# Optimization experiments

Measured on AMD Instinct MI355X. Metric: run time of the kernel, lower is better.

The kernel has to match this reference:

```python
import jax, jax.numpy as jnp
import numpy as np

N, H, R, E = 100000, 128, 30, 600000
EPS = 1e-5  # BatchNorm1d default eps


def _rgcn_layer(h, src, dst, etype, W, root, bias):
    """PyG RGCNConv: out = h @ root + bias + sum_r scatter_mean_r(h[src] @ W[r]).
    Mean is per (dst, relation) edge count."""
    n = h.shape[0]
    r_count = W.shape[0]
    seg = dst * r_count + etype                      # combined (dst, rel) segment id
    deg = jax.ops.segment_sum(jnp.ones_like(etype, dtype=h.dtype), seg,
                              num_segments=n * r_count)
    norm = 1.0 / jnp.maximum(deg[seg], 1.0)          # (E,) per-edge mean weight

    def body(out, inp):
        Wr, r = inp
        xr = h @ Wr                                  # (N,H) relation-transformed feats
        contrib = jnp.where((etype == r)[:, None], xr[src] * norm[:, None], 0.0)
        return out + jax.ops.segment_sum(contrib, dst, num_segments=n), None

    out0 = h @ root + bias
    out, _ = jax.lax.scan(body, out0, (W, jnp.arange(r_count)))
    return out


def _bn_relu(h, gamma, beta):
    # BatchNorm1d in training mode: biased batch statistics over the node dim
    mu = h.mean(axis=0)
    var = h.var(axis=0)
    return jax.nn.relu((h - mu) * jax.lax.rsqrt(var + EPS) * gamma + beta)


def setup_inputs() -> dict:
    key = jax.random.key(0)
    ks = jax.random.split(key, 16)
    s = 1.0 / np.sqrt(H)
    return {
        "x": jnp.arange(N, dtype=jnp.int32),
        "edge_index": jax.random.randint(ks[0], (2, E), 0, N, dtype=jnp.int32),
        "edge_type": jax.random.randint(ks[1], (E,), 0, R, dtype=jnp.int32),
        "emb": jax.random.normal(ks[2], (N, H), jnp.float32) * s,
        "W1": jax.random.normal(ks[3], (R, H, H), jnp.float32) * s,
        "root1": jax.random.normal(ks[4], (H, H), jnp.float32) * s,
        "b1": jnp.zeros((H,), jnp.float32),
        "g1": jnp.ones((H,), jnp.float32),
        "be1": jnp.zeros((H,), jnp.float32),
        "W2": jax.random.normal(ks[5], (R, H, H), jnp.float32) * s,
        "root2": jax.random.normal(ks[6], (H, H), jnp.float32) * s,
        "b2": jnp.zeros((H,), jnp.float32),
        "g2": jnp.ones((H,), jnp.float32),
        "be2": jnp.zeros((H,), jnp.float32),
    }


def reference(x, edge_index, edge_type, emb, W1, root1, b1, g1, be1,
              W2, root2, b2, g2, be2):
    src, dst = edge_index[0], edge_index[1]
    h = emb[x]                                        # (N,H) embedding lookup
    h = _bn_relu(_rgcn_layer(h, src, dst, edge_type, W1, root1, b1), g1, be1)
    h = _bn_relu(_rgcn_layer(h, src, dst, edge_type, W2, root2, b2), g2, be2)
    return h  # dropout is identity (deterministic reference)
```

## Files before the change

### kernel.cpp

```cpp
#include <hip/hip_runtime.h>
#include <hip/hip_bf16.h>

#define NN 100000
#define HH 128
#define RR 30
#define RR2 15
#define NE 600000
#define TILE 64
#define CH 64
#define EPAD (NE + RR * TILE)
#define NCHMAX (EPAD / TILE)
#define NB_PS ((NN + 255) / 256)
#define NBLK_BN 784
#define RPB_BN 128
#define BN_EPS 1e-5f

typedef __bf16 v8bf __attribute__((ext_vector_type(8)));
typedef float  v4f  __attribute__((ext_vector_type(4)));
typedef unsigned int v4u __attribute__((ext_vector_type(4)));

static __device__ __forceinline__ unsigned short f2b(float f) {
    unsigned int u = __float_as_uint(f);
    unsigned int r = (u + 0x7FFF + ((u >> 16) & 1)) >> 16;
    return (unsigned short)r;
}

static __device__ __forceinline__ unsigned int pk_bf16(float lo, float hi) {
    unsigned int r;
    asm("v_cvt_pk_bf16_f32 %0, %1, %2" : "=v"(r) : "v"(lo), "v"(hi));
    return r;
}

__global__ void k_hist(const int* __restrict__ dst, const int* __restrict__ et,
                       unsigned int* __restrict__ deg16, int* __restrict__ cnt) {
    __shared__ int lh[RR];
    int t = threadIdx.x;
    if (t < RR) lh[t] = 0;
    __syncthreads();
    int i = blockIdx.x * blockDim.x + t;
    if (i < NE) {
        int d = dst[i], r = et[i];
        atomicAdd(&deg16[(size_t)d * RR2 + (r >> 1)], 1u << ((r & 1) * 16));
        atomicAdd(&lh[r], 1);
    }
    __syncthreads();
    if (t < RR && lh[t]) atomicAdd(&cnt[t], lh[t]);
}

__global__ void k_degsum(const unsigned int* __restrict__ deg16,
                         int* __restrict__ cnt_d) {
    int d = blockIdx.x * blockDim.x + threadIdx.x;
    if (d >= NN) return;
    int s = 0;
#pragma unroll
    for (int r2 = 0; r2 < RR2; ++r2) {
        unsigned int v = deg16[(size_t)d * RR2 + r2];
        s += (int)(v & 0xffffu) + (int)(v >> 16);
    }
    cnt_d[d] = s;
}

__global__ void k_scan(const int* __restrict__ cnt, int* __restrict__ cursor,
                       int* __restrict__ totals,
                       int* __restrict__ src_s, int* __restrict__ dst_s,
                       float* __restrict__ norm_s, int* __restrict__ dpos_s,
                       int* __restrict__ chunk_rel, int need_dst) {
    __shared__ int off[RR + 1];
    if (threadIdx.x == 0) {
        int acc = 0;
        for (int r = 0; r < RR; ++r) {
            off[r] = acc;
            acc += (cnt[r] + TILE - 1) / TILE;
        }
        off[RR] = acc;
        totals[0] = acc * TILE;
    }
    __syncthreads();
    for (int r = 0; r < RR; ++r) {
        for (int c = off[r] + (int)threadIdx.x; c < off[r + 1]; c += blockDim.x)
            chunk_rel[c] = r;
        int begin = off[r] * TILE + cnt[r];
        int end   = off[r + 1] * TILE;
        for (int p = begin + (int)threadIdx.x; p < end; p += blockDim.x) {
            src_s[p] = 0; norm_s[p] = 0.f;
            dpos_s[p] = NE;
            if (need_dst) dst_s[p] = 0;
        }
    }
    if (threadIdx.x == 0)
        for (int r = 0; r < RR; ++r) cursor[r] = off[r] * TILE;
}

__global__ void k_psum1(const int* __restrict__ c, int* __restrict__ bsum) {
    __shared__ int sh[256];
    int i = blockIdx.x * 256 + threadIdx.x;
    sh[threadIdx.x] = (i < NN) ? c[i] : 0;
    __syncthreads();
    for (int s = 128; s > 0; s >>= 1) {
        if (threadIdx.x < s) sh[threadIdx.x] += sh[threadIdx.x + s];
        __syncthreads();
    }
    if (threadIdx.x == 0) bsum[blockIdx.x] = sh[0];
}

__global__ void k_psum2(int* __restrict__ bsum) {
    __shared__ int sh[512];
    int t = threadIdx.x;
    sh[t] = (t < NB_PS) ? bsum[t] : 0;
    __syncthreads();
    if (t == 0) {
        int acc = 0;
        for (int b = 0; b < NB_PS; ++b) { int v = sh[b]; sh[b] = acc; acc += v; }
    }
    __syncthreads();
    if (t < NB_PS) bsum[t] = sh[t];
}

__global__ void k_psum3(const int* __restrict__ c, const int* __restrict__ bscan,
                        int* __restrict__ off, int* __restrict__ cur) {
    __shared__ int sh[256];
    int t = threadIdx.x;
    int i = blockIdx.x * 256 + t;
    int v = (i < NN) ? c[i] : 0;
    sh[t] = v;
    __syncthreads();
    for (int s = 1; s < 256; s <<= 1) {
        int a = (t >= s) ? sh[t - s] : 0;
        __syncthreads();
        sh[t] += a;
        __syncthreads();
    }
    int excl = sh[t] - v + bscan[blockIdx.x];
    if (i < NN) { off[i] = excl; cur[i] = excl; }
    if (i == 0) off[NN] = NE;
}

__global__ void k_fillds2(const int* __restrict__ off, int* __restrict__ ds2) {
    int d = blockIdx.x * blockDim.x + threadIdx.x;
    if (d >= NN) return;
    int s = off[d], e = off[d + 1];
    for (int p = s; p < e; ++p) ds2[p] = d;
}

__global__ void k_scatter(const int* __restrict__ src, const int* __restrict__ dst,
                          const int* __restrict__ et,
                          const unsigned int* __restrict__ deg16,
                          int* __restrict__ cursor, int* __restrict__ cursor_dst,
                          int* __restrict__ src_s, int* __restrict__ dst_s,
                          float* __restrict__ norm_s, int* __restrict__ dpos_s,
                          int need_dst) {
    __shared__ int lh[RR];
    __shared__ int lbase[RR];
    int t = threadIdx.x;
    if (t < RR) lh[t] = 0;
    __syncthreads();
    int i = blockIdx.x * blockDim.x + t;
    int r = 0, d = 0, lrank = 0;
    bool valid = (i < NE);
    if (valid) {
        r = et[i]; d = dst[i];
        lrank = atomicAdd(&lh[r], 1);
    }
    __syncthreads();
    if (t < RR && lh[t]) lbase[t] = atomicAdd(&cursor[t], lh[t]);
    __syncthreads();
    if (valid) {
        int pos = lbase[r] + lrank;
        src_s[pos] = src[i];
        if (need_dst) dst_s[pos] = d;
        int dg = (int)((deg16[(size_t)d * RR2 + (r >> 1)] >> ((r & 1) * 16)) & 0xffffu);
        norm_s[pos] = 1.0f / (float)(dg > 1 ? dg : 1);
        dpos_s[pos] = atomicAdd(&cursor_dst[d], 1);
    }
}

__global__ void k_convW(const float* __restrict__ W, unsigned short* __restrict__ Wt,
                        int total) {
    int idx = blockIdx.x * blockDim.x + threadIdx.x;
    if (idx >= total) return;
    int m = idx / (HH * HH);
    int rem = idx % (HH * HH);
    int k = rem / HH, c = rem % HH;
    Wt[m * HH * HH + c * HH + k] = f2b(W[idx]);
}

__global__ void k_embed(const int* __restrict__ x, const float* __restrict__ emb,
                        unsigned int* __restrict__ hb2) {
    int idx = blockIdx.x * blockDim.x + threadIdx.x;
    if (idx >= NN * HH / 2) return;
    int i = idx >> 6;
    int j2 = (idx & 63) * 2;
    const float* p = emb + (size_t)x[i] * HH + j2;
    hb2[idx] = pk_bf16(p[0], p[1]);
}

__global__ __launch_bounds__(256) void k_rootgemm(const unsigned short* __restrict__ hb,
                                                  const unsigned short* __restrict__ rootT,
                                                  const float* __restrict__ bias,
                                                  float* __restrict__ tmp) {
    __shared__ __align__(16) unsigned short Xs[TILE][HH + 8];
    __shared__ __align__(16) unsigned short Ws[HH][HH + 8];
    int base = blockIdx.x * TILE;
    int t = threadIdx.x;

    {
        int l = t >> 2, lr = t & 3;
        int row = base + l;
        for (int i = 0; i < 4; ++i) {
            int g = lr + 4 * i;
            uint4 v = {0u, 0u, 0u, 0u};
            if (row < NN) v = *reinterpret_cast<const uint4*>(hb + (size_t)row * HH + g * 8);
            *reinterpret_cast<uint4*>(&Xs[l][g * 8]) = v;
        }
    }
    for (int i = 0; i < 8; ++i) {
        int idx = t + 256 * i;
        int row = idx >> 4, g = idx & 15;
        *reinterpret_cast<uint4*>(&Ws[row][g * 8]) =
            *reinterpret_cast<const uint4*>(rootT + row * HH + g * 8);
    }
    __syncthreads();

    int w = t >> 6, lane = t & 63;
    int lr16 = lane & 15, kg = lane >> 4;
    v4f acc[8];
    for (int n = 0; n < 8; ++n) acc[n] = (v4f){0.f, 0.f, 0.f, 0.f};
#pragma unroll
    for (int kk = 0; kk < 4; ++kk) {
        int k0 = kk * 32 + kg * 8;
        v8bf a = *reinterpret_cast<const v8bf*>(&Xs[w * 16 + lr16][k0]);
#pragma unroll
        for (int n = 0; n < 8; ++n) {
            v8bf b = *reinterpret_cast<const v8bf*>(&Ws[n * 16 + lr16][k0]);
            acc[n] = __builtin_amdgcn_mfma_f32_16x16x32_bf16(a, b, acc[n], 0, 0, 0);
        }
    }
#pragma unroll
    for (int n = 0; n < 8; ++n)
        for (int j = 0; j < 4; ++j) {
            int row = base + w * 16 + kg * 4 + j;
            int col = n * 16 + lr16;
            if (row < NN) tmp[(size_t)row * HH + col] = acc[n][j] + bias[col];
        }
}

__global__ __launch_bounds__(256) void k_edgegemm_x(const unsigned short* __restrict__ hb,
                                                    const unsigned short* __restrict__ Wt,
                                                    const int* __restrict__ src_s,
                                                    const int* __restrict__ chunk_rel,
                                                    const float* __restrict__ norm_s,
                                                    const int* __restrict__ dpos_s,
                                                    const int* __restrict__ totals,
                                                    unsigned short* __restrict__ xe) {
    int ebase = blockIdx.x * TILE;
    if (ebase >= totals[0]) return;
    __shared__ __align__(16) unsigned short S[HH * (HH + 8)];
    int t = threadIdx.x;
    int rel = chunk_rel[blockIdx.x];

    const unsigned short* Wr = Wt + (size_t)rel * HH * HH;
    for (int i = 0; i < 8; ++i) {
        int idx = t + 256 * i;
        int row = idx >> 4, g = idx & 15;
        *reinterpret_cast<uint4*>(&S[row * (HH + 8) + g * 8]) =
            *reinterpret_cast<const uint4*>(Wr + row * HH + g * 8);
    }

    int w = t >> 6, lane = t & 63;
    int lr16 = lane & 15, kg = lane >> 4;
    int slot = w * 16 + lr16;
    int srow = src_s[ebase + slot];
    float nrm = norm_s[ebase + slot];

    v8bf xf[4];
    const unsigned short* hrow = hb + (size_t)srow * HH + kg * 8;
#pragma unroll
    for (int kk = 0; kk < 4; ++kk)
        xf[kk] = *reinterpret_cast<const v8bf*>(hrow + kk * 32);

    __syncthreads();

    v4f acc[8];
#pragma unroll
    for (int n = 0; n < 8; ++n) acc[n] = (v4f){0.f, 0.f, 0.f, 0.f};
#pragma unroll
    for (int n = 0; n < 8; ++n)
#pragma unroll
        for (int kk = 0; kk < 4; ++kk) {
            v8bf wf = *reinterpret_cast<const v8bf*>(
                &S[(n * 16 + lr16) * (HH + 8) + kk * 32 + kg * 8]);
            acc[n] = __builtin_amdgcn_mfma_f32_16x16x32_bf16(wf, xf[kk], acc[n], 0, 0, 0);
        }

    __syncthreads();

    int c = slot & 7;
#pragma unroll
    for (int n = 0; n < 8; ++n) {
        unsigned int w0 = pk_bf16(acc[n][0] * nrm, acc[n][1] * nrm);
        unsigned int w1 = pk_bf16(acc[n][2] * nrm, acc[n][3] * nrm);
        unsigned long long p = (unsigned long long)w0 | ((unsigned long long)w1 << 32);
        int a = n * 4 + kg;
        int sw = (((a >> 1) ^ c) << 1) | (a & 1);
        *reinterpret_cast<unsigned long long*>(&S[slot * HH + sw * 4]) = p;
    }
    __syncthreads();
    {
        int l = t >> 2, lr = t & 3;
        size_t drow = (size_t)dpos_s[ebase + l];
        int cs = l & 7;
        unsigned short* orow = xe + drow * HH;
#pragma unroll
        for (int i = 0; i < 4; ++i) {
            int j = lr + 4 * i;
            v4u v = *reinterpret_cast<const v4u*>(&S[l * HH + (j ^ cs) * 8]);
            *reinterpret_cast<v4u*>(orow + j * 8) = v;
        }
    }
}

__global__ __launch_bounds__(256) void k_edgegemm_at(const unsigned short* __restrict__ hb,
                                                     const unsigned short* __restrict__ Wt,
                                                     const int* __restrict__ src_s,
                                                     const int* __restrict__ dst_s,
                                                     const int* __restrict__ chunk_rel,
                                                     const float* __restrict__ norm_s,
                                                     const int* __restrict__ totals,
                                                     float* __restrict__ tmp) {
    int ebase = blockIdx.x * TILE;
    if (ebase >= totals[0]) return;
    __shared__ __align__(16) unsigned short Xs[TILE][HH + 8];
    __shared__ __align__(16) unsigned short Ws[HH][HH + 8];
    __shared__ int   src_l[TILE];
    __shared__ int   dst_l[TILE];
    __shared__ float nrm_l[TILE];
    int t = threadIdx.x;
    if (t < TILE) {
        src_l[t] = src_s[ebase + t];
        dst_l[t] = dst_s[ebase + t];
        nrm_l[t] = norm_s[ebase + t];
    }
    int rel = chunk_rel[blockIdx.x];
    __syncthreads();
    {
        int l = t >> 2, lr = t & 3;
        int srow = src_l[l];
        for (int i = 0; i < 4; ++i) {
            int g = lr + 4 * i;
            *reinterpret_cast<uint4*>(&Xs[l][g * 8]) =
                *reinterpret_cast<const uint4*>(hb + (size_t)srow * HH + g * 8);
        }
    }
    const unsigned short* Wr = Wt + (size_t)rel * HH * HH;
    for (int i = 0; i < 8; ++i) {
        int idx = t + 256 * i;
        int row = idx >> 4, g = idx & 15;
        *reinterpret_cast<uint4*>(&Ws[row][g * 8]) =
            *reinterpret_cast<const uint4*>(Wr + row * HH + g * 8);
    }
    __syncthreads();
    int w = t >> 6, lane = t & 63;
    int lr16 = lane & 15, kg = lane >> 4;
    v4f acc[8];
    for (int n = 0; n < 8; ++n) acc[n] = (v4f){0.f, 0.f, 0.f, 0.f};
#pragma unroll
    for (int kk = 0; kk < 4; ++kk) {
        int k0 = kk * 32 + kg * 8;
        v8bf a = *reinterpret_cast<const v8bf*>(&Xs[w * 16 + lr16][k0]);
#pragma unroll
        for (int n = 0; n < 8; ++n) {
            v8bf b = *reinterpret_cast<const v8bf*>(&Ws[n * 16 + lr16][k0]);
            acc[n] = __builtin_amdgcn_mfma_f32_16x16x32_bf16(a, b, acc[n], 0, 0, 0);
        }
    }
#pragma unroll
    for (int n = 0; n < 8; ++n)
        for (int j = 0; j < 4; ++j) {
            int slot = w * 16 + kg * 4 + j;
            int col  = n * 16 + lr16;
            atomicAdd(&tmp[(size_t)dst_l[slot] * HH + col], acc[n][j] * nrm_l[slot]);
        }
}

__global__ __launch_bounds__(256) void k_aggseg(const unsigned int* __restrict__ xe32,
                                                const int* __restrict__ ds2,
                                                float* __restrict__ tmp) {
    int wid = (blockIdx.x * blockDim.x + threadIdx.x) >> 6;
    int lane = threadIdx.x & 63;
    if (wid >= NE / CH) return;
    int c0 = wid * CH;

    int dme = ds2[c0 + lane];
    int dpre = __shfl_up(dme, 1);
    if (lane == 0) dpre = (c0 == 0) ? -1 : ds2[c0 - 1];
    unsigned long long bmask = __ballot(dme != dpre);
    int dnext = (c0 + CH < NE) ? ds2[c0 + CH] : -1;

    int dcur = __shfl(dme, 0);
    bool fresh = (bmask & 1ull) != 0;
    float a0 = 0.f, a1 = 0.f;
    for (int q0 = 0; q0 < CH; q0 += 16) {
        unsigned int v[16];
#pragma unroll
        for (int j = 0; j < 16; ++j)
            v[j] = xe32[(size_t)(c0 + q0 + j) * 64 + lane];
#pragma unroll
        for (int j = 0; j < 16; ++j) {
            int q = q0 + j;
            if (q && ((bmask >> q) & 1ull)) {
                float* base = tmp + (size_t)dcur * HH + lane * 2;
                if (fresh) {
                    float2* b2 = reinterpret_cast<float2*>(base);
                    float2 o = *b2; o.x += a0; o.y += a1; *b2 = o;
                } else {
                    atomicAdd(base, a0);
                    atomicAdd(base + 1, a1);
                }
                a0 = 0.f; a1 = 0.f;
                dcur = __shfl(dme, q);
                fresh = true;
            }
            a0 += __uint_as_float(v[j] << 16);
            a1 += __uint_as_float(v[j] & 0xffff0000u);
        }
    }
    {
        bool endclean = (dnext != dcur);
        float* base = tmp + (size_t)dcur * HH + lane * 2;
        if (fresh && endclean) {
            float2* b2 = reinterpret_cast<float2*>(base);
            float2 o = *b2; o.x += a0; o.y += a1; *b2 = o;
        } else {
            atomicAdd(base, a0);
            atomicAdd(base + 1, a1);
        }
    }
}

__global__ __launch_bounds__(256) void k_bnsum1(const float* __restrict__ tmp,
                                                float* __restrict__ psum,
                                                float* __restrict__ psq) {
    int t = threadIdx.x;
    int rg = t >> 5, lane = t & 31;
    int base = blockIdx.x * RPB_BN;
    v4f s = {0.f, 0.f, 0.f, 0.f}, q = {0.f, 0.f, 0.f, 0.f};
#pragma unroll 4
    for (int i = 0; i < RPB_BN / 8; ++i) {
        int row = base + rg + 8 * i;
        if (row < NN) {
            v4f v = *reinterpret_cast<const v4f*>(tmp + (size_t)row * HH + lane * 4);
            s += v; q += v * v;
        }
    }
    __shared__ v4f shs[8][32], shq[8][32];
    shs[rg][lane] = s; shq[rg][lane] = q;
    __syncthreads();
    if (rg == 0) {
        v4f ts = shs[0][lane], tq = shq[0][lane];
#pragma unroll
        for (int k = 1; k < 8; ++k) { ts += shs[k][lane]; tq += shq[k][lane]; }
        int b = blockIdx.x;
#pragma unroll
        for (int j = 0; j < 4; ++j) {
            psum[(size_t)(lane * 4 + j) * NBLK_BN + b] = ts[j];
            psq [(size_t)(lane * 4 + j) * NBLK_BN + b] = tq[j];
        }
    }
}

__global__ void k_bnsum2(const float* __restrict__ psum, const float* __restrict__ psq,
                         const float* __restrict__ g, const float* __restrict__ be,
                         float* __restrict__ sc_g, float* __restrict__ shf_g) {
    __shared__ float ssum[HH], ssq[HH];
    int t = threadIdx.x;
    int col = t & 127;
    const float* row = ((t < 128) ? psum : psq) + (size_t)col * NBLK_BN;
    v4f a = {0.f, 0.f, 0.f, 0.f};
    for (int i = 0; i < NBLK_BN / 4; ++i)
        a += *reinterpret_cast<const v4f*>(row + i * 4);
    float acc = a[0] + a[1] + a[2] + a[3];
    if (t < 128) ssum[col] = acc; else ssq[col] = acc;
    __syncthreads();
    if (t < 128) {
        float inv_n = 1.0f / (float)NN;
        float mean = ssum[col] * inv_n;
        float var = ssq[col] * inv_n - mean * mean;
        float sc = g[col] * rsqrtf(var + BN_EPS);
        sc_g[col] = sc;
        shf_g[col] = be[col] - mean * sc;
    }
}

__global__ void k_bnapply(const float* __restrict__ tmp, const float* __restrict__ sc_g,
                          const float* __restrict__ shf_g,
                          unsigned short* __restrict__ hout,
                          float* __restrict__ fout, int write_bf16) {
    int idx = blockIdx.x * blockDim.x + threadIdx.x;
    if (idx >= NN * HH / 4) return;
    int c4 = (idx & 31) * 4;
    v4f v  = *reinterpret_cast<const v4f*>(tmp + (size_t)idx * 4);
    v4f sc = *reinterpret_cast<const v4f*>(sc_g + c4);
    v4f sh = *reinterpret_cast<const v4f*>(shf_g + c4);
    v4f r;
#pragma unroll
    for (int j = 0; j < 4; ++j) r[j] = fmaxf(v[j] * sc[j] + sh[j], 0.f);
    if (write_bf16) {
        uint2 u;
        u.x = pk_bf16(r[0], r[1]);
        u.y = pk_bf16(r[2], r[3]);
        *reinterpret_cast<uint2*>(hout + (size_t)idx * 4) = u;
    } else {
        *reinterpret_cast<v4f*>(fout + (size_t)idx * 4) = r;
    }
}

constexpr size_t OFF_DEG  = 0;
constexpr size_t OFF_HB   = OFF_DEG + (size_t)NN * RR2 * 4;
constexpr size_t OFF_TMP  = OFF_HB + (size_t)NN * HH * 2;
constexpr size_t OFF_W1T  = OFF_TMP + (size_t)NN * HH * 4;
constexpr size_t OFF_W2T  = OFF_W1T + (size_t)RR * HH * HH * 2;
constexpr size_t OFF_R1T  = OFF_W2T + (size_t)RR * HH * HH * 2;
constexpr size_t OFF_R2T  = OFF_R1T + (size_t)HH * HH * 2;
constexpr size_t OFF_SRCS = OFF_R2T + (size_t)HH * HH * 2;
constexpr size_t OFF_DSTS = OFF_SRCS + (size_t)EPAD * 4;
constexpr size_t OFF_NRMS = OFF_DSTS + (size_t)EPAD * 4;
constexpr size_t OFF_DPOS = OFF_NRMS + (size_t)EPAD * 4;
constexpr size_t OFF_DS2  = OFF_DPOS + (size_t)EPAD * 4;
constexpr size_t OFF_CREL = OFF_DS2 + (size_t)EPAD * 4;
constexpr size_t OFF_CNTD = OFF_CREL + ((size_t)NCHMAX * 4 + 255 & ~(size_t)255);
constexpr size_t OFF_OFFD = OFF_CNTD + ((size_t)(NN + 1) * 4 + 255 & ~(size_t)255);
constexpr size_t OFF_CURD = OFF_OFFD + ((size_t)(NN + 1) * 4 + 255 & ~(size_t)255);
constexpr size_t OFF_BSUM = OFF_CURD + ((size_t)NN * 4 + 255 & ~(size_t)255);
constexpr size_t OFF_CTRL = OFF_BSUM + ((size_t)NB_PS * 4 + 255 & ~(size_t)255);
constexpr size_t OFF_SC   = OFF_CTRL + 512;
constexpr size_t OFF_SHF  = OFF_SC + 512;
constexpr size_t OFF_PSUM = OFF_SHF + 512;
constexpr size_t OFF_PSQ  = OFF_PSUM + (size_t)HH * NBLK_BN * 4;
constexpr size_t OFF_XE   = (OFF_PSQ + (size_t)HH * NBLK_BN * 4 + 255) & ~(size_t)255;
constexpr size_t WS_MIN   = OFF_XE;
constexpr size_t WS_FULL  = OFF_XE + (size_t)EPAD * HH * 2;

extern "C" void kernel_launch(void* const* d_in, const int* in_sizes, int n_in,
                              void* d_out, int out_size, void* d_ws, size_t ws_size,
                              hipStream_t stream) {
    const int*   x     = (const int*)d_in[0];
    const int*   eidx  = (const int*)d_in[1];
    const int*   et    = (const int*)d_in[2];
    const float* emb   = (const float*)d_in[3];
    const float* W1    = (const float*)d_in[4];
    const float* root1 = (const float*)d_in[5];
    const float* b1    = (const float*)d_in[6];
    const float* g1    = (const float*)d_in[7];
    const float* be1   = (const float*)d_in[8];
    const float* W2    = (const float*)d_in[9];
    const float* root2 = (const float*)d_in[10];
    const float* b2    = (const float*)d_in[11];
    const float* g2    = (const float*)d_in[12];
    const float* be2   = (const float*)d_in[13];
    float* out = (float*)d_out;

    if (ws_size < WS_MIN) return;
    const bool full = (ws_size >= WS_FULL);
    const int need_dst = full ? 0 : 1;

    char* ws = (char*)d_ws;
    unsigned int* deg16 = (unsigned int*)(ws + OFF_DEG);
    unsigned short* hb = (unsigned short*)(ws + OFF_HB);
    float* tmp    = (float*)(ws + OFF_TMP);
    unsigned short* W1t = (unsigned short*)(ws + OFF_W1T);
    unsigned short* W2t = (unsigned short*)(ws + OFF_W2T);
    unsigned short* r1t = (unsigned short*)(ws + OFF_R1T);
    unsigned short* r2t = (unsigned short*)(ws + OFF_R2T);
    int*   src_s  = (int*)(ws + OFF_SRCS);
    int*   dst_s  = (int*)(ws + OFF_DSTS);
    float* norm_s = (float*)(ws + OFF_NRMS);
    int*   dpos_s = (int*)(ws + OFF_DPOS);
    int*   ds2    = (int*)(ws + OFF_DS2);
    int*   crel   = (int*)(ws + OFF_CREL);
    int*   cnt_d  = (int*)(ws + OFF_CNTD);
    int*   off_d  = (int*)(ws + OFF_OFFD);
    int*   cur_d  = (int*)(ws + OFF_CURD);
    int*   bsum   = (int*)(ws + OFF_BSUM);
    int*   cnt    = (int*)(ws + OFF_CTRL);
    int*   cursor = cnt + 32;
    int*   totals = cnt + 64;
    float* sc_g   = (float*)(ws + OFF_SC);
    float* shf_g  = (float*)(ws + OFF_SHF);
    float* psum   = (float*)(ws + OFF_PSUM);
    float* psq    = (float*)(ws + OFF_PSQ);
    unsigned short* xe = (unsigned short*)(ws + OFF_XE);

    const int* srcp = eidx;
    const int* dstp = eidx + NE;

    hipMemsetAsync(deg16, 0, (size_t)NN * RR2 * 4, stream);
    hipMemsetAsync(cnt, 0, 512, stream);

    k_hist<<<(NE + 255) / 256, 256, 0, stream>>>(dstp, et, deg16, cnt);
    k_degsum<<<(NN + 255) / 256, 256, 0, stream>>>(deg16, cnt_d);
    k_scan<<<1, 256, 0, stream>>>(cnt, cursor, totals, src_s, dst_s, norm_s,
                                  dpos_s, crel, need_dst);
    k_psum1<<<NB_PS, 256, 0, stream>>>(cnt_d, bsum);
    k_psum2<<<1, 512, 0, stream>>>(bsum);
    k_psum3<<<NB_PS, 256, 0, stream>>>(cnt_d, bsum, off_d, cur_d);
    k_fillds2<<<(NN + 255) / 256, 256, 0, stream>>>(off_d, ds2);
    k_scatter<<<(NE + 255) / 256, 256, 0, stream>>>(srcp, dstp, et, deg16, cursor, cur_d,
                                                    src_s, dst_s, norm_s, dpos_s,
                                                    need_dst);
    k_convW<<<(RR * HH * HH + 255) / 256, 256, 0, stream>>>(W1, W1t, RR * HH * HH);
    k_convW<<<(RR * HH * HH + 255) / 256, 256, 0, stream>>>(W2, W2t, RR * HH * HH);
    k_convW<<<(HH * HH + 255) / 256, 256, 0, stream>>>(root1, r1t, HH * HH);
    k_convW<<<(HH * HH + 255) / 256, 256, 0, stream>>>(root2, r2t, HH * HH);
    k_embed<<<(NN * HH / 2 + 255) / 256, 256, 0, stream>>>(x, emb, (unsigned int*)hb);

    const unsigned short* Wts[2] = {W1t, W2t};
    const unsigned short* rts[2] = {r1t, r2t};
    const float* biases[2] = {b1, b2};
    const float* gs[2]     = {g1, g2};
    const float* bes[2]    = {be1, be2};

    const int nchunks = NE / CH;
    for (int layer = 0; layer < 2; ++layer) {
        k_rootgemm<<<(NN + TILE - 1) / TILE, 256, 0, stream>>>(hb, rts[layer],
                                                               biases[layer], tmp);
        if (full) {
            k_edgegemm_x<<<EPAD / TILE, 256, 0, stream>>>(hb, Wts[layer], src_s, crel,
                                                          norm_s, dpos_s, totals, xe);
            k_aggseg<<<(nchunks + 3) / 4, 256, 0, stream>>>((const unsigned int*)xe,
                                                            ds2, tmp);
        } else {
            k_edgegemm_at<<<EPAD / TILE, 256, 0, stream>>>(hb, Wts[layer], src_s, dst_s,
                                                           crel, norm_s, totals, tmp);
        }
        k_bnsum1<<<NBLK_BN, 256, 0, stream>>>(tmp, psum, psq);
        k_bnsum2<<<1, 256, 0, stream>>>(psum, psq, gs[layer], bes[layer], sc_g, shf_g);
        k_bnapply<<<(NN * HH / 4 + 255) / 256, 256, 0, stream>>>(tmp, sc_g, shf_g,
                                                                 hb, out, layer == 0);
    }
}
```

Before: 508.0 us.

## Fuse root GEMM with CSR segment aggregation, removing atomics and ds2 fill

Replaces the separate root GEMM and the atomic segmented aggregation with one kernel. Each block computes the root transform for 64 destination rows with MFMA, then walks each row's CSR range of per-edge transformed features and adds them in registers before a single store with bias. This removes the ds2 fill kernel, one full read-modify-write pass over the fp32 output, and the atomics. The per-row edge loops are serial and uneven in length, and each thread reads strided 8-byte pieces of xe, which may coalesce less well.

Result: faster. 485.2 us (-4.5%).

```diff
diff --git a/kernel.cpp b/kernel.cpp
--- a/kernel.cpp
+++ b/kernel.cpp
@@ -7,7 +7,6 @@
 #define RR2 15
 #define NE 600000
 #define TILE 64
-#define CH 64
 #define EPAD (NE + RR * TILE)
 #define NCHMAX (EPAD / TILE)
 #define NB_PS ((NN + 255) / 256)
@@ -135,13 +134,6 @@
     if (i == 0) off[NN] = NE;
 }
 
-__global__ void k_fillds2(const int* __restrict__ off, int* __restrict__ ds2) {
-    int d = blockIdx.x * blockDim.x + threadIdx.x;
-    if (d >= NN) return;
-    int s = off[d], e = off[d + 1];
-    for (int p = s; p < e; ++p) ds2[p] = d;
-}
-
 __global__ void k_scatter(const int* __restrict__ src, const int* __restrict__ dst,
                           const int* __restrict__ et,
                           const unsigned int* __restrict__ deg16,
@@ -192,6 +184,73 @@
     int j2 = (idx & 63) * 2;
     const float* p = emb + (size_t)x[i] * HH + j2;
     hb2[idx] = pk_bf16(p[0], p[1]);
+}
+
+__global__ __launch_bounds__(256) void k_rootagg(const unsigned short* __restrict__ hb,
+                                                 const unsigned short* __restrict__ rootT,
+                                                 const float* __restrict__ bias,
+                                                 const int* __restrict__ off,
+                                                 const unsigned short* __restrict__ xe,
+                                                 float* __restrict__ tmp) {
+    __shared__ __align__(16) unsigned short Ws[HH][HH + 8];
+    int t = threadIdx.x;
+    int base = blockIdx.x * TILE;
+
+    for (int i = 0; i < 8; ++i) {
+        int idx = t + 256 * i;
+        int row = idx >> 4, g = idx & 15;
+        *reinterpret_cast<uint4*>(&Ws[row][g * 8]) =
+            *reinterpret_cast<const uint4*>(rootT + row * HH + g * 8);
+    }
+
+    int w = t >> 6, lane = t & 63;
+    int lr16 = lane & 15, kg = lane >> 4;
+    int slot = w * 16 + lr16;
+    int drow = base + slot;
+    bool valid = (drow < NN);
+    int dsafe = valid ? drow : 0;
+
+    v8bf xf[4];
+    const unsigned short* hrow = hb + (size_t)dsafe * HH + kg * 8;
+#pragma unroll
+    for (int kk = 0; kk < 4; ++kk)
+        xf[kk] = *reinterpret_cast<const v8bf*>(hrow + kk * 32);
+
+    __syncthreads();
+
+    v4f acc[8];
+#pragma unroll
+    for (int n = 0; n < 8; ++n) acc[n] = (v4f){0.f, 0.f, 0.f, 0.f};
+#pragma unroll
+    for (int n = 0; n < 8; ++n)
+#pragma unroll
+        for (int kk = 0; kk < 4; ++kk) {
+            v8bf wf = *reinterpret_cast<const v8bf*>(&Ws[n * 16 + lr16][kk * 32 + kg * 8]);
+            acc[n] = __builtin_amdgcn_mfma_f32_16x16x32_bf16(wf, xf[kk], acc[n], 0, 0, 0);
+        }
+
+    int s = valid ? off[drow] : 0;
+    int e = valid ? off[drow + 1] : 0;
+    for (int p = s; p < e; ++p) {
+        const unsigned short* xr = xe + (size_t)p * HH + kg * 4;
+#pragma unroll
+        for (int n = 0; n < 8; ++n) {
+            uint2 u = *reinterpret_cast<const uint2*>(xr + n * 16);
+            acc[n][0] += __uint_as_float(u.x << 16);
+            acc[n][1] += __uint_as_float(u.x & 0xffff0000u);
+            acc[n][2] += __uint_as_float(u.y << 16);
+            acc[n][3] += __uint_as_float(u.y & 0xffff0000u);
+        }
+    }
+
+    if (valid) {
+        float* orow = tmp + (size_t)drow * HH + kg * 4;
+#pragma unroll
+        for (int n = 0; n < 8; ++n) {
+            v4f b = *reinterpret_cast<const v4f*>(bias + n * 16 + kg * 4);
+            *reinterpret_cast<v4f*>(orow + n * 16) = acc[n] + b;
+        }
+    }
 }
 
 __global__ __launch_bounds__(256) void k_rootgemm(const unsigned short* __restrict__ hb,
@@ -382,61 +441,6 @@
         }
 }
 
-__global__ __launch_bounds__(256) void k_aggseg(const unsigned int* __restrict__ xe32,
-                                                const int* __restrict__ ds2,
-                                                float* __restrict__ tmp) {
-    int wid = (blockIdx.x * blockDim.x + threadIdx.x) >> 6;
-    int lane = threadIdx.x & 63;
-    if (wid >= NE / CH) return;
-    int c0 = wid * CH;
-
-    int dme = ds2[c0 + lane];
-    int dpre = __shfl_up(dme, 1);
-    if (lane == 0) dpre = (c0 == 0) ? -1 : ds2[c0 - 1];
-    unsigned long long bmask = __ballot(dme != dpre);
-    int dnext = (c0 + CH < NE) ? ds2[c0 + CH] : -1;
-
-    int dcur = __shfl(dme, 0);
-    bool fresh = (bmask & 1ull) != 0;
-    float a0 = 0.f, a1 = 0.f;
-    for (int q0 = 0; q0 < CH; q0 += 16) {
-        unsigned int v[16];
-#pragma unroll
-        for (int j = 0; j < 16; ++j)
-            v[j] = xe32[(size_t)(c0 + q0 + j) * 64 + lane];
-#pragma unroll
-        for (int j = 0; j < 16; ++j) {
-            int q = q0 + j;
-            if (q && ((bmask >> q) & 1ull)) {
-                float* base = tmp + (size_t)dcur * HH + lane * 2;
-                if (fresh) {
-                    float2* b2 = reinterpret_cast<float2*>(base);
-                    float2 o = *b2; o.x += a0; o.y += a1; *b2 = o;
-                } else {
-                    atomicAdd(base, a0);
-                    atomicAdd(base + 1, a1);
-                }
-                a0 = 0.f; a1 = 0.f;
-                dcur = __shfl(dme, q);
-                fresh = true;
-            }
-            a0 += __uint_as_float(v[j] << 16);
-            a1 += __uint_as_float(v[j] & 0xffff0000u);
-        }
-    }
-    {
-        bool endclean = (dnext != dcur);
-        float* base = tmp + (size_t)dcur * HH + lane * 2;
-        if (fresh && endclean) {
-            float2* b2 = reinterpret_cast<float2*>(base);
-            float2 o = *b2; o.x += a0; o.y += a1; *b2 = o;
-        } else {
-            atomicAdd(base, a0);
-            atomicAdd(base + 1, a1);
-        }
-    }
-}
-
 __global__ __launch_bounds__(256) void k_bnsum1(const float* __restrict__ tmp,
                                                 float* __restrict__ psum,
                                                 float* __restrict__ psq) {
@@ -525,8 +529,7 @@
 constexpr size_t OFF_DSTS = OFF_SRCS + (size_t)EPAD * 4;
 constexpr size_t OFF_NRMS = OFF_DSTS + (size_t)EPAD * 4;
 constexpr size_t OFF_DPOS = OFF_NRMS + (size_t)EPAD * 4;
-constexpr size_t OFF_DS2  = OFF_DPOS + (size_t)EPAD * 4;
-constexpr size_t OFF_CREL = OFF_DS2 + (size_t)EPAD * 4;
+constexpr size_t OFF_CREL = OFF_DPOS + (size_t)EPAD * 4;
 constexpr size_t OFF_CNTD = OFF_CREL + ((size_t)NCHMAX * 4 + 255 & ~(size_t)255);
 constexpr size_t OFF_OFFD = OFF_CNTD + ((size_t)(NN + 1) * 4 + 255 & ~(size_t)255);
 constexpr size_t OFF_CURD = OFF_OFFD + ((size_t)(NN + 1) * 4 + 255 & ~(size_t)255);
@@ -575,7 +578,6 @@
     int*   dst_s  = (int*)(ws + OFF_DSTS);
     float* norm_s = (float*)(ws + OFF_NRMS);
     int*   dpos_s = (int*)(ws + OFF_DPOS);
-    int*   ds2    = (int*)(ws + OFF_DS2);
     int*   crel   = (int*)(ws + OFF_CREL);
     int*   cnt_d  = (int*)(ws + OFF_CNTD);
     int*   off_d  = (int*)(ws + OFF_OFFD);
@@ -603,7 +605,6 @@
     k_psum1<<<NB_PS, 256, 0, stream>>>(cnt_d, bsum);
     k_psum2<<<1, 512, 0, stream>>>(bsum);
     k_psum3<<<NB_PS, 256, 0, stream>>>(cnt_d, bsum, off_d, cur_d);
-    k_fillds2<<<(NN + 255) / 256, 256, 0, stream>>>(off_d, ds2);
     k_scatter<<<(NE + 255) / 256, 256, 0, stream>>>(srcp, dstp, et, deg16, cursor, cur_d,
                                                     src_s, dst_s, norm_s, dpos_s,
                                                     need_dst);
@@ -619,16 +620,16 @@
     const float* gs[2]     = {g1, g2};
     const float* bes[2]    = {be1, be2};
 
-    const int nchunks = NE / CH;
     for (int layer = 0; layer < 2; ++layer) {
-        k_rootgemm<<<(NN + TILE - 1) / TILE, 256, 0, stream>>>(hb, rts[layer],
-                                                               biases[layer], tmp);
         if (full) {
             k_edgegemm_x<<<EPAD / TILE, 256, 0, stream>>>(hb, Wts[layer], src_s, crel,
                                                           norm_s, dpos_s, totals, xe);
-            k_aggseg<<<(nchunks + 3) / 4, 256, 0, stream>>>((const unsigned int*)xe,
-                                                            ds2, tmp);
+            k_rootagg<<<(NN + TILE - 1) / TILE, 256, 0, stream>>>(hb, rts[layer],
+                                                                  biases[layer], off_d,
+                                                                  xe, tmp);
         } else {
+            k_rootgemm<<<(NN + TILE - 1) / TILE, 256, 0, stream>>>(hb, rts[layer],
+                                                                   biases[layer], tmp);
             k_edgegemm_at<<<EPAD / TILE, 256, 0, stream>>>(hb, Wts[layer], src_s, dst_s,
                                                            crel, norm_s, totals, tmp);
         }
```
